# Kernel optimization log

Hardware: AMD Instinct MI355X
Metric: run time of the kernel (lower is better)

Reference implementation:

```python
import jax, jax.numpy as jnp
import numpy as np

D_MODEL = 2048
NUM_HEADS = 16
D_K = D_MODEL // NUM_HEADS
BASE = 10000.0


def rotate_half(x):
    half = x.shape[-1] // 2
    x1, x2 = x[..., :half], x[..., half:]
    return jnp.concatenate((-x2, x1), axis=-1)


def setup_inputs() -> dict:
    key = jax.random.key(0)
    ks = jax.random.split(key, 9)
    B, S = 2, 2048
    std = 1.0 / np.sqrt(D_MODEL)
    inp = {"x": jax.random.normal(ks[0], (B, S, D_MODEL), dtype=jnp.float32)}
    for i, name in enumerate(["q", "k", "v", "o"]):
        inp[f"w_{name}"] = jax.random.uniform(ks[1 + i], (D_MODEL, D_MODEL), jnp.float32, -std, std)
        inp[f"b_{name}"] = jax.random.uniform(ks[5 + i], (D_MODEL,), jnp.float32, -std, std)
    return inp


def reference(x, w_q, b_q, w_k, b_k, w_v, b_v, w_o, b_o):
    B, S, _ = x.shape
    # projections -> (B, H, S, d_k)
    def proj(w, b):
        y = x @ w.T + b
        return y.reshape(B, S, NUM_HEADS, D_K).transpose(0, 2, 1, 3)
    Q, K, V = proj(w_q, b_q), proj(w_k, b_k), proj(w_v, b_v)
    # rotary embeddings
    inv_freq = 1.0 / (BASE ** (jnp.arange(0, D_K, 2, dtype=jnp.float32) / D_K))
    t = jnp.arange(S, dtype=jnp.float32)
    freqs = jnp.einsum("i,j->ij", t, inv_freq)  # (S, d_k/2)
    emb = jnp.concatenate((freqs, freqs), axis=-1)  # (S, d_k)
    cos, sin = jnp.cos(emb), jnp.sin(emb)
    Q = Q * cos + rotate_half(Q) * sin
    K = K * cos + rotate_half(K) * sin
    # attention
    scores = jnp.einsum("bhqd,bhkd->bhqk", Q, K) / np.sqrt(D_K).astype(np.float32)
    attn = jax.nn.softmax(scores, axis=-1)  # dropout p=0 (eval)
    out = jnp.einsum("bhqk,bhkd->bhqd", attn, V)
    out = out.transpose(0, 2, 1, 3).reshape(B, S, D_MODEL)
    return out @ w_o.T + b_o
```

## Files before the change

### kernel.cpp

```cpp
#include <hip/hip_runtime.h>
#include <hip/hip_bf16.h>
#include <math.h>


#define D_MODEL 2048
#define NHEADS  16
#define DK      128
#define BATCH   2
#define SEQ     2048
#define MTOT    (BATCH*SEQ)
#define XN      (MTOT*D_MODEL)
#define WN      (D_MODEL*D_MODEL)

typedef __attribute__((ext_vector_type(8))) short bf16x8;
typedef __attribute__((ext_vector_type(4))) float f32x4;
typedef __attribute__((ext_vector_type(8))) unsigned short u16x8;

__device__ __forceinline__ float bf2f(unsigned short u) {
    union { unsigned int i; float f; } v; v.i = ((unsigned int)u) << 16; return v.f;
}
__device__ __forceinline__ unsigned short f2bfu(float f) {
    __hip_bfloat16 h = __float2bfloat16(f);
    return *reinterpret_cast<unsigned short*>(&h);
}
__device__ __forceinline__ void async_copy16(const unsigned short* g, unsigned short* l) {
    __builtin_amdgcn_global_load_lds((const __attribute__((address_space(1))) void*)g,
                                     (__attribute__((address_space(3))) void*)l, 16, 0, 0);
}

__global__ void rope_table_kernel(float2* __restrict__ cs) {
    int idx = blockIdx.x * blockDim.x + threadIdx.x;
    if (idx >= SEQ * 64) return;
    int s = idx >> 6, j = idx & 63;
    double inv = pow(10000.0, -(double)j / 64.0);
    double f = (double)s * inv;
    cs[idx] = make_float2((float)cos(f), (float)sin(f));
}

__global__ void convert_kernel(const float* __restrict__ x,
                               const float* __restrict__ wq, const float* __restrict__ wk,
                               const float* __restrict__ wv, const float* __restrict__ wo,
                               unsigned short* __restrict__ Xbf, unsigned short* __restrict__ Wbf) {
    size_t e = ((size_t)blockIdx.x * blockDim.x + threadIdx.x) * 4;
    const float* src; unsigned short* dst;
    if (e < XN) { src = x + e; dst = Xbf + e; }
    else {
        size_t r = e - XN; int w = (int)(r >> 22); size_t o = r & (WN - 1);
        src = (w == 0 ? wq : w == 1 ? wk : w == 2 ? wv : wo) + o;
        dst = Wbf + (size_t)w * WN + o;
    }
    float4 v = *(const float4*)src;
    ushort4 u;
    u.x = f2bfu(v.x); u.y = f2bfu(v.y); u.z = f2bfu(v.z); u.w = f2bfu(v.w);
    *(ushort4*)dst = u;
}

#define BM 128
#define BN 128
#define BK 32

template<int AMODE, int CMODE>
__global__ __launch_bounds__(256, 2)
void gemm_bf16_kernel(const unsigned short* __restrict__ A,
                      const unsigned short* __restrict__ W,
                      const float* __restrict__ bias, void* __restrict__ Cout) {
    __shared__ unsigned short smem[8192];
    const int tid = threadIdx.x;
    const int lane = tid & 63, wid = tid >> 6;
    const int wm = wid >> 1, wn = wid & 1;
    const int m0 = blockIdx.x * BM, n0 = blockIdx.y * BN;

    f32x4 acc[4][4];
    #pragma unroll
    for (int i = 0; i < 4; ++i)
        #pragma unroll
        for (int j = 0; j < 4; ++j) acc[i][j] = (f32x4){0.f, 0.f, 0.f, 0.f};

    const int lrow = lane & 15, lkc = lane >> 4;

    for (int k0 = 0; k0 < D_MODEL; k0 += BK) {
        #pragma unroll
        for (int i = 0; i < 4; ++i) {
            const int off = i * 4096 + wid * 1024 + lane * 16;
            const unsigned short* src;
            if (i < 2) {
                int elem = off >> 1, row = elem >> 5, col = elem & 31;
                if (AMODE == 0) {
                    src = A + (size_t)(m0 + row) * D_MODEL + k0 + col;
                } else {
                    int m = m0 + row, b = m >> 11, s = m & 2047;
                    src = A + (((size_t)(b * NHEADS + (k0 >> 7))) * SEQ + s) * DK + (k0 & 127) + col;
                }
            } else {
                int elem = (off - 8192) >> 1, row = elem >> 5, col = elem & 31;
                src = W + (size_t)(n0 + row) * D_MODEL + k0 + col;
            }
            async_copy16(src, &smem[(i * 4096 + wid * 1024) >> 1]);
        }
        __syncthreads();

        bf16x8 a[4], b[4];
        #pragma unroll
        for (int mi = 0; mi < 4; ++mi)
            a[mi] = *(const bf16x8*)&smem[(wm * 64 + mi * 16 + lrow) * 32 + lkc * 8];
        #pragma unroll
        for (int ni = 0; ni < 4; ++ni)
            b[ni] = *(const bf16x8*)&smem[4096 + (wn * 64 + ni * 16 + lrow) * 32 + lkc * 8];
        #pragma unroll
        for (int mi = 0; mi < 4; ++mi)
            #pragma unroll
            for (int ni = 0; ni < 4; ++ni)
                acc[mi][ni] = __builtin_amdgcn_mfma_f32_16x16x32_bf16(a[mi], b[ni], acc[mi][ni], 0, 0, 0);
        __syncthreads();
    }

    const int lq = lane >> 4;
    #pragma unroll
    for (int ni = 0; ni < 4; ++ni) {
        int col = n0 + wn * 64 + ni * 16 + lrow;
        float bv = bias[col];
        #pragma unroll
        for (int mi = 0; mi < 4; ++mi) {
            #pragma unroll
            for (int r = 0; r < 4; ++r) {
                int row = m0 + wm * 64 + mi * 16 + lq * 4 + r;
                float v = acc[mi][ni][r] + bv;
                if (CMODE == 0) {
                    ((float*)Cout)[(size_t)row * D_MODEL + col] = v;
                } else {
                    int bb = row >> 11, s = row & 2047, h = col >> 7, d = col & 127;
                    ((unsigned short*)Cout)[(((size_t)(bb * NHEADS + h)) * SEQ + s) * DK + d] = f2bfu(v);
                }
            }
        }
    }
}

__global__ void rope_kernel(unsigned short* __restrict__ Q, unsigned short* __restrict__ Kt,
                            const float2* __restrict__ cs) {
    const float qscale = 0.08838834764831845f;
    int idx = blockIdx.x * blockDim.x + threadIdx.x;
    if (idx >= BATCH * NHEADS * SEQ * 8) return;
    int j8 = idx & 7, bhs = idx >> 3, s = bhs & (SEQ - 1);
    int d0 = j8 * 8;
    size_t base = (size_t)bhs * DK;
    u16x8 qlo = *(const u16x8*)(Q + base + d0);
    u16x8 qhi = *(const u16x8*)(Q + base + 64 + d0);
    u16x8 klo = *(const u16x8*)(Kt + base + d0);
    u16x8 khi = *(const u16x8*)(Kt + base + 64 + d0);
    u16x8 olo, ohi, plo, phi;
    #pragma unroll
    for (int j = 0; j < 8; ++j) {
        float2 c = cs[(s << 6) + d0 + j];
        float q0 = bf2f(qlo[j]), q1 = bf2f(qhi[j]);
        olo[j] = f2bfu((q0 * c.x - q1 * c.y) * qscale);
        ohi[j] = f2bfu((q1 * c.x + q0 * c.y) * qscale);
        float k0 = bf2f(klo[j]), k1 = bf2f(khi[j]);
        plo[j] = f2bfu(k0 * c.x - k1 * c.y);
        phi[j] = f2bfu(k1 * c.x + k0 * c.y);
    }
    *(u16x8*)(Q + base + d0) = olo;
    *(u16x8*)(Q + base + 64 + d0) = ohi;
    *(u16x8*)(Kt + base + d0) = plo;
    *(u16x8*)(Kt + base + 64 + d0) = phi;
}

#define AQT 64
#define AKT 64
#define VSS 72
#define PSS 72

__global__ __launch_bounds__(256, 3)
void attn_mfma_kernel(unsigned short* __restrict__ Q,
                      const unsigned short* __restrict__ Kp,
                      const unsigned short* __restrict__ Vp) {
    __shared__ unsigned short Ks[AKT * DK];
    __shared__ unsigned short Vs[DK * VSS];
    __shared__ unsigned short Ps[AQT * PSS];
    const int tid = threadIdx.x;
    const int lane = tid & 63, wid = tid >> 6;
    const int lrow = lane & 15, lkc = lane >> 4;
    const int bh = blockIdx.y;
    const int q0 = blockIdx.x * AQT;
    unsigned short* qpanel = Q + (size_t)bh * SEQ * DK;
    const unsigned short* kpanel = Kp + (size_t)bh * SEQ * DK;
    const unsigned short* vpanel = Vp + (size_t)bh * SEQ * DK;

    bf16x8 qfrag[4];
    {
        const unsigned short* qsrc = qpanel + (size_t)(q0 + wid * 16 + lrow) * DK + lkc * 8;
        #pragma unroll
        for (int c = 0; c < 4; ++c)
            qfrag[c] = *(const bf16x8*)(qsrc + c * 32);
    }

    float m_i[4], l_i[4];
    f32x4 oacc[8];
    #pragma unroll
    for (int r = 0; r < 4; ++r) { m_i[r] = -1e30f; l_i[r] = 0.f; }
    #pragma unroll
    for (int dt = 0; dt < 8; ++dt) oacc[dt] = (f32x4){0.f, 0.f, 0.f, 0.f};

    const int v_kk = lane;
    const int v_d0 = wid * 32;

    for (int kv0 = 0; kv0 < SEQ; kv0 += AKT) {
        __syncthreads();
        #pragma unroll
        for (int i = 0; i < 4; ++i) {
            int dstByte = i * 4096 + wid * 1024 + lane * 16;
            int elem = dstByte >> 1;
            int row = elem >> 7, col = elem & 127;
            int colS = col ^ ((row & 7) << 3);
            async_copy16(kpanel + (size_t)(kv0 + row) * DK + colS,
                         &Ks[i * 2048 + wid * 512]);
        }
        {
            const unsigned short* src = vpanel + (size_t)(kv0 + v_kk) * DK + v_d0;
            u16x8 a0 = *(const u16x8*)(src);
            u16x8 a1 = *(const u16x8*)(src + 8);
            u16x8 a2 = *(const u16x8*)(src + 16);
            u16x8 a3 = *(const u16x8*)(src + 24);
            #pragma unroll
            for (int j = 0; j < 8; ++j) {
                Vs[(v_d0 + j)      * VSS + v_kk] = a0[j];
                Vs[(v_d0 + 8 + j)  * VSS + v_kk] = a1[j];
                Vs[(v_d0 + 16 + j) * VSS + v_kk] = a2[j];
                Vs[(v_d0 + 24 + j) * VSS + v_kk] = a3[j];
            }
        }
        __syncthreads();

        f32x4 sacc[4];
        #pragma unroll
        for (int t = 0; t < 4; ++t) sacc[t] = (f32x4){0.f, 0.f, 0.f, 0.f};
        #pragma unroll
        for (int t = 0; t < 4; ++t) {
            int krl = t * 16 + lrow;
            int sw = (krl & 7) << 3;
            #pragma unroll
            for (int c = 0; c < 4; ++c) {
                bf16x8 kf = *(const bf16x8*)&Ks[(krl * DK + c * 32 + lkc * 8) ^ sw];
                sacc[t] = __builtin_amdgcn_mfma_f32_16x16x32_bf16(qfrag[c], kf, sacc[t], 0, 0, 0);
            }
        }

        float mx[4];
        #pragma unroll
        for (int r = 0; r < 4; ++r) {
            float v = fmaxf(fmaxf(sacc[0][r], sacc[1][r]), fmaxf(sacc[2][r], sacc[3][r]));
            #pragma unroll
            for (int off = 1; off <= 8; off <<= 1)
                v = fmaxf(v, __shfl_xor(v, off, 64));
            mx[r] = v;
        }
        int cond = (mx[0] - m_i[0] <= 8.f) && (mx[1] - m_i[1] <= 8.f) &&
                   (mx[2] - m_i[2] <= 8.f) && (mx[3] - m_i[3] <= 8.f);
        if (!__all(cond)) {
            #pragma unroll
            for (int r = 0; r < 4; ++r) {
                float mnew = fmaxf(m_i[r], mx[r]);
                float corr = __expf(m_i[r] - mnew);
                l_i[r] *= corr;
                #pragma unroll
                for (int dt = 0; dt < 8; ++dt) oacc[dt][r] *= corr;
                m_i[r] = mnew;
            }
        }
        #pragma unroll
        for (int r = 0; r < 4; ++r) {
            float p0 = __expf(sacc[0][r] - m_i[r]);
            float p1 = __expf(sacc[1][r] - m_i[r]);
            float p2 = __expf(sacc[2][r] - m_i[r]);
            float p3 = __expf(sacc[3][r] - m_i[r]);
            float rs = (p0 + p1) + (p2 + p3);
            #pragma unroll
            for (int off = 1; off <= 8; off <<= 1)
                rs += __shfl_xor(rs, off, 64);
            l_i[r] += rs;
            int pb = (wid * 16 + lkc * 4 + r) * PSS;
            Ps[pb + lrow]      = f2bfu(p0);
            Ps[pb + 16 + lrow] = f2bfu(p1);
            Ps[pb + 32 + lrow] = f2bfu(p2);
            Ps[pb + 48 + lrow] = f2bfu(p3);
        }

        const int arow = (wid * 16 + lrow) * PSS;
        bf16x8 pfA = *(const bf16x8*)&Ps[arow + lkc * 8];
        bf16x8 pfB = *(const bf16x8*)&Ps[arow + 32 + lkc * 8];
        #pragma unroll
        for (int dt = 0; dt < 8; ++dt) {
            int db = (dt * 16 + lrow) * VSS;
            bf16x8 vfA = *(const bf16x8*)&Vs[db + lkc * 8];
            bf16x8 vfB = *(const bf16x8*)&Vs[db + 32 + lkc * 8];
            oacc[dt] = __builtin_amdgcn_mfma_f32_16x16x32_bf16(pfA, vfA, oacc[dt], 0, 0, 0);
            oacc[dt] = __builtin_amdgcn_mfma_f32_16x16x32_bf16(pfB, vfB, oacc[dt], 0, 0, 0);
        }
    }

    float inv[4];
    #pragma unroll
    for (int r = 0; r < 4; ++r) inv[r] = 1.0f / l_i[r];
    #pragma unroll
    for (int dt = 0; dt < 8; ++dt) {
        #pragma unroll
        for (int r = 0; r < 4; ++r) {
            int q = q0 + wid * 16 + lkc * 4 + r;
            qpanel[(size_t)q * DK + dt * 16 + lrow] = f2bfu(oacc[dt][r] * inv[r]);
        }
    }
}

extern "C" void kernel_launch(void* const* d_in, const int* in_sizes, int n_in,
                              void* d_out, int out_size, void* d_ws, size_t ws_size,
                              hipStream_t stream) {
    const float* x   = (const float*)d_in[0];
    const float* w_q = (const float*)d_in[1];
    const float* b_q = (const float*)d_in[2];
    const float* w_k = (const float*)d_in[3];
    const float* b_k = (const float*)d_in[4];
    const float* w_v = (const float*)d_in[5];
    const float* b_v = (const float*)d_in[6];
    const float* w_o = (const float*)d_in[7];
    const float* b_o = (const float*)d_in[8];
    float* out = (float*)d_out;

    char* ws = (char*)d_ws;
    const size_t bfTensor = (size_t)BATCH * NHEADS * SEQ * DK * 2;
    unsigned short* Qbf = (unsigned short*)(ws);
    unsigned short* Kbf = (unsigned short*)(ws + bfTensor);
    unsigned short* Vbf = (unsigned short*)(ws + 2 * bfTensor);
    unsigned short* Xbf = (unsigned short*)(ws + 3 * bfTensor);
    unsigned short* Wbf = (unsigned short*)(ws + 4 * bfTensor);
    float2*         cs  = (float2*)(ws + 6 * bfTensor);

    rope_table_kernel<<<(SEQ * 64 + 255) / 256, 256, 0, stream>>>(cs);
    convert_kernel<<<(XN + 4 * WN) / 4 / 256, 256, 0, stream>>>(x, w_q, w_k, w_v, w_o, Xbf, Wbf);

    dim3 ggrid(MTOT / BM, D_MODEL / BN);
    gemm_bf16_kernel<0, 1><<<ggrid, 256, 0, stream>>>(Xbf, Wbf + 0 * (size_t)WN, b_q, Qbf);
    gemm_bf16_kernel<0, 1><<<ggrid, 256, 0, stream>>>(Xbf, Wbf + 1 * (size_t)WN, b_k, Kbf);
    gemm_bf16_kernel<0, 1><<<ggrid, 256, 0, stream>>>(Xbf, Wbf + 2 * (size_t)WN, b_v, Vbf);

    rope_kernel<<<(BATCH * NHEADS * SEQ * 8 + 255) / 256, 256, 0, stream>>>(Qbf, Kbf, cs);

    attn_mfma_kernel<<<dim3(SEQ / AQT, BATCH * NHEADS), 256, 0, stream>>>(Qbf, Kbf, Vbf);

    gemm_bf16_kernel<1, 0><<<ggrid, 256, 0, stream>>>(Qbf, Wbf + 3 * (size_t)WN, b_o, out);
}
```

Baseline: 539.5 us.

## Write V transposed from projection GEMM and double-buffer K/V async loads in attention

```diff
diff --git a/kernel.cpp b/kernel.cpp
--- a/kernel.cpp
+++ b/kernel.cpp
@@ -64,7 +64,7 @@
 void gemm_bf16_kernel(const unsigned short* __restrict__ A,
                       const unsigned short* __restrict__ W,
                       const float* __restrict__ bias, void* __restrict__ Cout) {
-    __shared__ unsigned short smem[8192];
+    __shared__ unsigned short smem[8704];
     const int tid = threadIdx.x;
     const int lane = tid & 63, wid = tid >> 6;
     const int wm = wid >> 1, wn = wid & 1;
@@ -115,23 +115,60 @@
     }
 
     const int lq = lane >> 4;
-    #pragma unroll
-    for (int ni = 0; ni < 4; ++ni) {
-        int col = n0 + wn * 64 + ni * 16 + lrow;
-        float bv = bias[col];
-        #pragma unroll
-        for (int mi = 0; mi < 4; ++mi) {
-            #pragma unroll
-            for (int r = 0; r < 4; ++r) {
-                int row = m0 + wm * 64 + mi * 16 + lq * 4 + r;
-                float v = acc[mi][ni][r] + bv;
-                if (CMODE == 0) {
-                    ((float*)Cout)[(size_t)row * D_MODEL + col] = v;
-                } else {
-                    int bb = row >> 11, s = row & 2047, h = col >> 7, d = col & 127;
-                    ((unsigned short*)Cout)[(((size_t)(bb * NHEADS + h)) * SEQ + s) * DK + d] = f2bfu(v);
+    if (CMODE != 2) {
+        #pragma unroll
+        for (int ni = 0; ni < 4; ++ni) {
+            int col = n0 + wn * 64 + ni * 16 + lrow;
+            float bv = bias[col];
+            #pragma unroll
+            for (int mi = 0; mi < 4; ++mi) {
+                #pragma unroll
+                for (int r = 0; r < 4; ++r) {
+                    int row = m0 + wm * 64 + mi * 16 + lq * 4 + r;
+                    float v = acc[mi][ni][r] + bv;
+                    if (CMODE == 0) {
+                        ((float*)Cout)[(size_t)row * D_MODEL + col] = v;
+                    } else {
+                        int bb = row >> 11, s = row & 2047, h = col >> 7, d = col & 127;
+                        ((unsigned short*)Cout)[(((size_t)(bb * NHEADS + h)) * SEQ + s) * DK + d] = f2bfu(v);
+                    }
                 }
             }
+        }
+    } else {
+        const int b = m0 >> 11;
+        const int h = n0 >> 7;
+        const int sbase = m0 & 2047;
+        unsigned short* vtbase = (unsigned short*)Cout +
+            (((size_t)(b * NHEADS + h)) * DK) * SEQ + sbase;
+        #pragma unroll
+        for (int half = 0; half < 2; ++half) {
+            __syncthreads();
+            if (wn == half) {
+                #pragma unroll
+                for (int ni = 0; ni < 4; ++ni) {
+                    float bv = bias[n0 + half * 64 + ni * 16 + lrow];
+                    #pragma unroll
+                    for (int mi = 0; mi < 4; ++mi)
+                        #pragma unroll
+                        for (int r = 0; r < 4; ++r) {
+                            int row = wm * 64 + mi * 16 + lq * 4 + r;
+                            smem[row * 68 + ni * 16 + lrow] = f2bfu(acc[mi][ni][r] + bv);
+                        }
+                }
+            }
+            __syncthreads();
+            int dl = tid >> 2, s0 = (tid & 3) * 32;
+            u16x8 o[4];
+            #pragma unroll
+            for (int j8 = 0; j8 < 4; ++j8)
+                #pragma unroll
+                for (int j = 0; j < 8; ++j)
+                    o[j8][j] = smem[(s0 + j8 * 8 + j) * 68 + dl];
+            unsigned short* dst = vtbase + (size_t)(half * 64 + dl) * SEQ + s0;
+            #pragma unroll
+            for (int j8 = 0; j8 < 4; ++j8)
+                *(u16x8*)(dst + j8 * 8) = o[j8];
         }
     }
 }
@@ -167,15 +204,15 @@
 
 #define AQT 64
 #define AKT 64
-#define VSS 72
+#define NT  (SEQ/AKT)
 #define PSS 72
 
-__global__ __launch_bounds__(256, 3)
+__global__ __launch_bounds__(256, 2)
 void attn_mfma_kernel(unsigned short* __restrict__ Q,
                       const unsigned short* __restrict__ Kp,
-                      const unsigned short* __restrict__ Vp) {
-    __shared__ unsigned short Ks[AKT * DK];
-    __shared__ unsigned short Vs[DK * VSS];
+                      const unsigned short* __restrict__ VTp) {
+    __shared__ unsigned short Ks[2][AKT * DK];
+    __shared__ unsigned short Vs[2][DK * AKT];
     __shared__ unsigned short Ps[AQT * PSS];
     const int tid = threadIdx.x;
     const int lane = tid & 63, wid = tid >> 6;
@@ -183,8 +220,8 @@
     const int bh = blockIdx.y;
     const int q0 = blockIdx.x * AQT;
     unsigned short* qpanel = Q + (size_t)bh * SEQ * DK;
-    const unsigned short* kpanel = Kp + (size_t)bh * SEQ * DK;
-    const unsigned short* vpanel = Vp + (size_t)bh * SEQ * DK;
+    const unsigned short* kpanel  = Kp  + (size_t)bh * SEQ * DK;
+    const unsigned short* vtpanel = VTp + (size_t)bh * DK * SEQ;
 
     bf16x8 qfrag[4];
     {
@@ -194,6 +231,31 @@
             qfrag[c] = *(const bf16x8*)(qsrc + c * 32);
     }
 
+    const int st_elem = wid * 512 + lane * 8;
+    const int k_row = st_elem >> 7;
+    const int k_colS = ((st_elem & 127)) ;
+    const int v_d = st_elem >> 6;
+    const int v_c = (st_elem >> 3) & 7;
+
+#define STAGE(tt, bb)                                                                   \
+    {                                                                                   \
+        int kv0 = (tt) * AKT;                                                           \
+        _Pragma("unroll")                                                               \
+        for (int i = 0; i < 4; ++i) {                                                   \
+            int row = i * 16 + k_row;                                                   \
+            int colS = k_colS ^ ((row & 7) << 3);                                       \
+            async_copy16(kpanel + (size_t)(kv0 + row) * DK + colS,                      \
+                         &Ks[bb][i * 2048 + wid * 512]);                                \
+        }                                                                               \
+        _Pragma("unroll")                                                               \
+        for (int i = 0; i < 4; ++i) {                                                   \
+            int d = i * 32 + v_d;                                                       \
+            int cS = v_c ^ (d & 7);                                                     \
+            async_copy16(vtpanel + (size_t)d * SEQ + kv0 + cS * 8,                      \
+                         &Vs[bb][i * 2048 + wid * 512]);                                \
+        }                                                                               \
+    }
+
     float m_i[4], l_i[4];
     f32x4 oacc[8];
     #pragma unroll
@@ -201,35 +263,21 @@
     #pragma unroll
     for (int dt = 0; dt < 8; ++dt) oacc[dt] = (f32x4){0.f, 0.f, 0.f, 0.f};
 
-    const int v_kk = lane;
-    const int v_d0 = wid * 32;
-
-    for (int kv0 = 0; kv0 < SEQ; kv0 += AKT) {
-        __syncthreads();
-        #pragma unroll
-        for (int i = 0; i < 4; ++i) {
-            int dstByte = i * 4096 + wid * 1024 + lane * 16;
-            int elem = dstByte >> 1;
-            int row = elem >> 7, col = elem & 127;
-            int colS = col ^ ((row & 7) << 3);
-            async_copy16(kpanel + (size_t)(kv0 + row) * DK + colS,
-                         &Ks[i * 2048 + wid * 512]);
-        }
-        {
-            const unsigned short* src = vpanel + (size_t)(kv0 + v_kk) * DK + v_d0;
-            u16x8 a0 = *(const u16x8*)(src);
-            u16x8 a1 = *(const u16x8*)(src + 8);
-            u16x8 a2 = *(const u16x8*)(src + 16);
-            u16x8 a3 = *(const u16x8*)(src + 24);
-            #pragma unroll
-            for (int j = 0; j < 8; ++j) {
-                Vs[(v_d0 + j)      * VSS + v_kk] = a0[j];
-                Vs[(v_d0 + 8 + j)  * VSS + v_kk] = a1[j];
-                Vs[(v_d0 + 16 + j) * VSS + v_kk] = a2[j];
-                Vs[(v_d0 + 24 + j) * VSS + v_kk] = a3[j];
-            }
-        }
-        __syncthreads();
+    STAGE(0, 0);
+    int buf = 0;
+
+    for (int tt = 0; tt < NT; ++tt) {
+        if (tt + 1 < NT) {
+            STAGE(tt + 1, buf ^ 1);
+            asm volatile("s_waitcnt vmcnt(8)" ::: "memory");
+        } else {
+            asm volatile("s_waitcnt vmcnt(0)" ::: "memory");
+        }
+        __builtin_amdgcn_sched_barrier(0);
+        __builtin_amdgcn_s_barrier();
+
+        const unsigned short* KsB = Ks[buf];
+        const unsigned short* VsB = Vs[buf];
 
         f32x4 sacc[4];
         #pragma unroll
@@ -240,7 +288,7 @@
             int sw = (krl & 7) << 3;
             #pragma unroll
             for (int c = 0; c < 4; ++c) {
-                bf16x8 kf = *(const bf16x8*)&Ks[(krl * DK + c * 32 + lkc * 8) ^ sw];
+                bf16x8 kf = *(const bf16x8*)&KsB[(krl * DK + c * 32 + lkc * 8) ^ sw];
                 sacc[t] = __builtin_amdgcn_mfma_f32_16x16x32_bf16(qfrag[c], kf, sacc[t], 0, 0, 0);
             }
         }
@@ -290,13 +338,20 @@
         bf16x8 pfB = *(const bf16x8*)&Ps[arow + 32 + lkc * 8];
         #pragma unroll
         for (int dt = 0; dt < 8; ++dt) {
-            int db = (dt * 16 + lrow) * VSS;
-            bf16x8 vfA = *(const bf16x8*)&Vs[db + lkc * 8];
-            bf16x8 vfB = *(const bf16x8*)&Vs[db + 32 + lkc * 8];
+            int d = dt * 16 + lrow;
+            int basev = d * 64;
+            bf16x8 vfA = *(const bf16x8*)&VsB[basev + ((lkc     ^ (lrow & 7)) * 8)];
+            bf16x8 vfB = *(const bf16x8*)&VsB[basev + (((lkc+4) ^ (lrow & 7)) * 8)];
             oacc[dt] = __builtin_amdgcn_mfma_f32_16x16x32_bf16(pfA, vfA, oacc[dt], 0, 0, 0);
             oacc[dt] = __builtin_amdgcn_mfma_f32_16x16x32_bf16(pfB, vfB, oacc[dt], 0, 0, 0);
         }
-    }
+
+        asm volatile("s_waitcnt lgkmcnt(0)" ::: "memory");
+        __builtin_amdgcn_sched_barrier(0);
+        __builtin_amdgcn_s_barrier();
+        buf ^= 1;
+    }
+#undef STAGE
 
     float inv[4];
     #pragma unroll
@@ -327,12 +382,12 @@
 
     char* ws = (char*)d_ws;
     const size_t bfTensor = (size_t)BATCH * NHEADS * SEQ * DK * 2;
-    unsigned short* Qbf = (unsigned short*)(ws);
-    unsigned short* Kbf = (unsigned short*)(ws + bfTensor);
-    unsigned short* Vbf = (unsigned short*)(ws + 2 * bfTensor);
-    unsigned short* Xbf = (unsigned short*)(ws + 3 * bfTensor);
-    unsigned short* Wbf = (unsigned short*)(ws + 4 * bfTensor);
-    float2*         cs  = (float2*)(ws + 6 * bfTensor);
+    unsigned short* Qbf  = (unsigned short*)(ws);
+    unsigned short* Kbf  = (unsigned short*)(ws + bfTensor);
+    unsigned short* VTbf = (unsigned short*)(ws + 2 * bfTensor);
+    unsigned short* Xbf  = (unsigned short*)(ws + 3 * bfTensor);
+    unsigned short* Wbf  = (unsigned short*)(ws + 4 * bfTensor);
+    float2*         cs   = (float2*)(ws + 6 * bfTensor);
 
     rope_table_kernel<<<(SEQ * 64 + 255) / 256, 256, 0, stream>>>(cs);
     convert_kernel<<<(XN + 4 * WN) / 4 / 256, 256, 0, stream>>>(x, w_q, w_k, w_v, w_o, Xbf, Wbf);
@@ -340,11 +395,11 @@
     dim3 ggrid(MTOT / BM, D_MODEL / BN);
     gemm_bf16_kernel<0, 1><<<ggrid, 256, 0, stream>>>(Xbf, Wbf + 0 * (size_t)WN, b_q, Qbf);
     gemm_bf16_kernel<0, 1><<<ggrid, 256, 0, stream>>>(Xbf, Wbf + 1 * (size_t)WN, b_k, Kbf);
-    gemm_bf16_kernel<0, 1><<<ggrid, 256, 0, stream>>>(Xbf, Wbf + 2 * (size_t)WN, b_v, Vbf);
+    gemm_bf16_kernel<0, 2><<<ggrid, 256, 0, stream>>>(Xbf, Wbf + 2 * (size_t)WN, b_v, VTbf);
 
     rope_kernel<<<(BATCH * NHEADS * SEQ * 8 + 255) / 256, 256, 0, stream>>>(Qbf, Kbf, cs);
 
-    attn_mfma_kernel<<<dim3(SEQ / AQT, BATCH * NHEADS), 256, 0, stream>>>(Qbf, Kbf, Vbf);
+    attn_mfma_kernel<<<dim3(SEQ / AQT, BATCH * NHEADS), 256, 0, stream>>>(Qbf, Kbf, VTbf);
 
     gemm_bf16_kernel<1, 0><<<ggrid, 256, 0, stream>>>(Qbf, Wbf + 3 * (size_t)WN, b_o, out);
 }
```

Result: faster. 508.5 us (-5.7%).
